# Optimization experiments

Hardware: AMD Instinct MI355X
Metric: run time of the kernel (lower is better)

Reference implementation:

```python
import jax, jax.numpy as jnp
import numpy as np

BSZ, L, P, H = 8, 8192, 128, 128


def setup_inputs() -> dict:
    key = jax.random.key(0)
    ks = jax.random.split(key, 7)
    x = jax.random.normal(ks[0], (BSZ, L, H), jnp.float32)
    A_diag = jax.random.uniform(ks[1], (P,), jnp.float32, 0.0, 2.0)
    G_diag = jax.random.uniform(ks[2], (P,), jnp.float32, 0.0, 1.0)
    dt = jax.random.normal(ks[3], (P,), jnp.float32)
    B = jax.random.uniform(ks[4], (P, H, 2), jnp.float32, -1.0, 1.0) / np.sqrt(H)
    C = jax.random.uniform(ks[5], (H, P, 2), jnp.float32, -1.0, 1.0) / np.sqrt(P)
    D = jax.random.normal(ks[6], (H,), jnp.float32)
    return {"x": x, "A_diag": A_diag, "G_diag": G_diag, "dt": dt, "B": B, "C": C, "D": D}


def _project_G(G, A, dt):
    # clamp G >= 0 and fold A into the valid stability interval [A_low, A_high]
    G = jnp.maximum(G, 0.0)
    dt2 = jnp.maximum(dt ** 2, 1e-06)
    s = jnp.sqrt(1.0 + dt * G)
    A_low = (2.0 + dt * G - 2.0 * s) / dt2
    A_high = (2.0 + dt * G + 2.0 * s) / dt2
    A_proj = A_low + jax.nn.relu(A - A_low) - jax.nn.relu(A - A_high)
    return A_proj, G


def _binop(q_i, q_j):
    # 2x2 block (per diagonal state p) recurrence composition: M_j @ M_i
    A_i, b_i = q_i
    A_j, b_j = q_j
    A_new = jnp.einsum('...ikp,...kjp->...ijp', A_j, A_i)
    b_new = jnp.einsum('...ikp,...kp->...ip', A_j, b_i) + b_j
    return A_new, b_new


def reference(x, A_diag, G_diag, dt, B, C, D):
    # _project_A_dt
    dt_s = jax.nn.sigmoid(dt)                       # (P,)
    A = jnp.maximum(A_diag, 0.0)
    # G_base = projected G given (A, dt)
    _, G_base = _project_G(G_diag, A, dt_s)
    # constant damping: G_seq is G_base broadcast over time, then re-projected per step
    G_seq = jnp.broadcast_to(G_base, (L, P))        # (L,P)
    A_seq, G_seq = _project_G(G_seq, A, dt_s)       # broadcasts over L
    A_fin = jnp.min(A_seq, axis=0)                  # (P,)
    # complex input projection Bu_k = B_complex @ u_k
    Bc = B[..., 0] + 1j * B[..., 1]                 # (P,H)
    Cc = C[..., 0] + 1j * C[..., 1]                 # (H,P)
    Bu = jnp.einsum('blh,ph->blp', x, Bc)           # (BSZ,L,P) complex64
    # IMEX transition coefficients
    S = 1.0 + dt_s * G_seq                          # (L,P)
    M11 = 1.0 / S
    M12 = -(dt_s / S) * A_fin
    M21 = dt_s / S
    M22 = 1.0 - (dt_s ** 2 / S) * A_fin
    M = jnp.stack([jnp.stack([M11, M12], axis=-2),
                   jnp.stack([M21, M22], axis=-2)], axis=-3)   # (L,2,2,P) real
    F = jnp.stack([(dt_s / S) * Bu, (dt_s ** 2 / S) * Bu], axis=-2)  # (BSZ,L,2,P) complex
    M_b = jnp.broadcast_to(M, (BSZ,) + M.shape)     # (BSZ,L,2,2,P)
    _, xs = jax.lax.associative_scan(_binop, (M_b, F), axis=1)
    ys = xs[..., 1, :]                              # (BSZ,L,P) complex: x-component
    out = jnp.einsum('blp,hp->blh', ys, Cc).real + D * x
    return out
```

## Files before the change

### kernel.cpp

```cpp
#include <hip/hip_runtime.h>
#include <math.h>

#define BSZ_ 8
#define LEN_ 8192
#define NC_  128
#define CT_  64

typedef __attribute__((ext_vector_type(8))) short bf16x8;
typedef __attribute__((ext_vector_type(4))) float f32x4;

#define OFF_PRM 0
#define OFF_W1T 2048
#define OFF_W2T (OFF_W1T + 16384)
#define OFF_SUM (OFF_W2T + 16384)

__device__ __forceinline__ unsigned short f2bf(float f) {
    unsigned u = __builtin_bit_cast(unsigned, f);
    u += 0x7fffu + ((u >> 16) & 1u);
    return (unsigned short)(u >> 16);
}

__global__ __launch_bounds__(256) void k_setup(const float* __restrict__ A_diag,
                                               const float* __restrict__ G_diag,
                                               const float* __restrict__ dt,
                                               const float* __restrict__ B,
                                               const float* __restrict__ C,
                                               float* __restrict__ ws)
{
    int i = blockIdx.x * 256 + threadIdx.x;
    {
        int pc = i >> 7, h = i & 127;
        int p = pc >> 1, cc = pc & 1;
        float dts = 1.f / (1.f + expf(-dt[p]));
        float G = fmaxf(G_diag[p], 0.f);
        float c1 = dts / (1.f + dts * G);
        ((unsigned short*)(ws + OFF_W1T))[i] = f2bf(c1 * B[p * 256 + h * 2 + cc]);
    }
    {
        float v = C[i];
        ((unsigned short*)(ws + OFF_W2T))[i] = f2bf((i & 1) ? -v : v);
    }
    if (blockIdx.x == 0 && threadIdx.x < 128) {
        int p = threadIdx.x;
        float dtv = dt[p];
        float dts = 1.f / (1.f + expf(-dtv));
        float A   = fmaxf(A_diag[p], 0.f);
        float G   = fmaxf(G_diag[p], 0.f);
        float dt2 = fmaxf(dts * dts, 1e-6f);
        float s   = sqrtf(1.f + dts * G);
        float A_low  = (2.f + dts * G - 2.f * s) / dt2;
        float A_high = (2.f + dts * G + 2.f * s) / dt2;
        float Af = A_low + fmaxf(A - A_low, 0.f) - fmaxf(A - A_high, 0.f);
        float S   = 1.f + dts * G;
        float M11 = 1.f / S;
        float M12 = -(dts / S) * Af;
        float M21 = dts / S;
        float M22 = 1.f - (dts * dts / S) * Af;
        float t11 = M11, t12 = M12, t21 = M21, t22 = M22;
#pragma unroll
        for (int it = 0; it < 6; ++it) {
            float n11 = t11 * t11 + t12 * t21;
            float n12 = t11 * t12 + t12 * t22;
            float n21 = t21 * t11 + t22 * t21;
            float n22 = t21 * t12 + t22 * t22;
            t11 = n11; t12 = n12; t21 = n21; t22 = n22;
        }
        float* prm = ws + OFF_PRM + p * 16;
        prm[0] = M11; prm[1] = M12; prm[2] = M21; prm[3] = M22; prm[4] = dts;
        prm[5] = t11; prm[6] = t12; prm[7] = t21; prm[8] = t22;
    }
}

__device__ __forceinline__ void stage_x(const float* __restrict__ X, size_t row0,
                                        int tid, unsigned short (*xs)[136])
{
    int r = tid >> 4, cl = (tid & 15) * 8;
#pragma unroll
    for (int i = 0; i < 4; ++i) {
        int rr = r + i * 16;
        const float* src = X + (row0 + rr) * 128 + cl;
        float4 v0 = *(const float4*)src;
        float4 v1 = *(const float4*)(src + 4);
        unsigned short* dst = &xs[rr][cl];
        dst[0] = f2bf(v0.x); dst[1] = f2bf(v0.y); dst[2] = f2bf(v0.z); dst[3] = f2bf(v0.w);
        dst[4] = f2bf(v1.x); dst[5] = f2bf(v1.y); dst[6] = f2bf(v1.z); dst[7] = f2bf(v1.w);
    }
}

__device__ __forceinline__ void gemm1_acc(const unsigned short (*xs)[136],
                                          const unsigned short* __restrict__ W1T,
                                          int wv, int lane, f32x4 acc[4][4])
{
    int l15 = lane & 15, quad = lane >> 4;
    int nbase = wv * 64;
#pragma unroll
    for (int kk = 0; kk < 4; ++kk) {
        int k0 = kk * 32 + quad * 8;
        bf16x8 af[4], bg[4];
#pragma unroll
        for (int mi = 0; mi < 4; ++mi) af[mi] = *(const bf16x8*)&xs[mi * 16 + l15][k0];
#pragma unroll
        for (int nj = 0; nj < 4; ++nj)
            bg[nj] = *(const bf16x8*)(W1T + (size_t)(nbase + nj * 16 + l15) * 128 + k0);
#pragma unroll
        for (int mi = 0; mi < 4; ++mi)
#pragma unroll
            for (int nj = 0; nj < 4; ++nj)
                acc[mi][nj] = __builtin_amdgcn_mfma_f32_16x16x32_bf16(af[mi], bg[nj], acc[mi][nj], 0, 0, 0);
    }
}

__global__ __launch_bounds__(256) void k_fuse1(const float* __restrict__ X,
                                               float* __restrict__ ws)
{
    __shared__ __align__(16) char smem[64 * 258 * 4];
    unsigned short (*xs)[136] = (unsigned short (*)[136])smem;
    float (*fl)[258] = (float (*)[258])smem;

    int tid = threadIdx.x;
    int b = blockIdx.x >> 7, c = blockIdx.x & 127;
    size_t row0 = (size_t)b * LEN_ + (size_t)c * CT_;

    stage_x(X, row0, tid, xs);
    __syncthreads();

    int wv = tid >> 6, lane = tid & 63;
    int l15 = lane & 15, quad = lane >> 4, nbase = wv * 64;
    f32x4 acc[4][4] = {};
    gemm1_acc(xs, (const unsigned short*)(ws + OFF_W1T), wv, lane, acc);
    __syncthreads();

#pragma unroll
    for (int mi = 0; mi < 4; ++mi)
#pragma unroll
        for (int nj = 0; nj < 4; ++nj)
#pragma unroll
            for (int r = 0; r < 4; ++r)
                fl[mi * 16 + quad * 4 + r][nbase + nj * 16 + l15] = acc[mi][nj][r];
    __syncthreads();

    const float* prm = ws + OFF_PRM + (tid >> 1) * 16;
    float M11 = prm[0], M12 = prm[1], M21 = prm[2], M22 = prm[3], dts = prm[4];
    float h1 = 0.f, h2 = 0.f;
#pragma unroll 8
    for (int t = 0; t < CT_; ++t) {
        float u = fl[t][tid];
        float n1 = fmaf(M11, h1, fmaf(M12, h2, u));
        float n2 = fmaf(M21, h1, fmaf(M22, h2, dts * u));
        h1 = n1; h2 = n2;
    }
    *(float2*)(ws + OFF_SUM + (((size_t)b * NC_ + c) * 256 + tid) * 2) = make_float2(h1, h2);
}

__global__ __launch_bounds__(64) void k_scan2(float* __restrict__ ws)
{
    int b = blockIdx.x >> 2, cg = blockIdx.x & 3;
    int ch = cg * 64 + threadIdx.x;
    const float* prm = ws + OFF_PRM + (ch >> 1) * 16;
    float T11 = prm[5], T12 = prm[6], T21 = prm[7], T22 = prm[8];
    float e1 = 0.f, e2 = 0.f;
    float* base = ws + OFF_SUM + (size_t)b * 65536 + ch * 2;
#pragma unroll 8
    for (int j = 0; j < NC_; ++j) {
        float2 l = *(float2*)(base + (size_t)j * 512);
        *(float2*)(base + (size_t)j * 512) = make_float2(e1, e2);
        float n1 = fmaf(T11, e1, fmaf(T12, e2, l.x));
        float n2 = fmaf(T21, e1, fmaf(T22, e2, l.y));
        e1 = n1; e2 = n2;
    }
}

__global__ __launch_bounds__(256) void k_fuse2(const float* __restrict__ X,
                                               const float* __restrict__ Dv,
                                               float* __restrict__ ws,
                                               float* __restrict__ out)
{
    __shared__ __align__(16) char smem[64 * 260 * 4];
    unsigned short (*xs)[136] = (unsigned short (*)[136])smem;
    float (*fl)[260]          = (float (*)[260])smem;
    __shared__ __align__(16) unsigned short ysb[64][264];

    int tid = threadIdx.x;
    int b = blockIdx.x >> 7, c = blockIdx.x & 127;
    size_t row0 = (size_t)b * LEN_ + (size_t)c * CT_;

    stage_x(X, row0, tid, xs);
    __syncthreads();

    int wv = tid >> 6, lane = tid & 63;
    int l15 = lane & 15, quad = lane >> 4, nbase = wv * 64;
    {
        f32x4 acc[4][4] = {};
        gemm1_acc(xs, (const unsigned short*)(ws + OFF_W1T), wv, lane, acc);
        __syncthreads();
#pragma unroll
        for (int mi = 0; mi < 4; ++mi)
#pragma unroll
            for (int nj = 0; nj < 4; ++nj)
#pragma unroll
                for (int r = 0; r < 4; ++r)
                    fl[mi * 16 + quad * 4 + r][nbase + nj * 16 + l15] = acc[mi][nj][r];
    }
    __syncthreads();

    {
        const float* prm = ws + OFF_PRM + (tid >> 1) * 16;
        float M11 = prm[0], M12 = prm[1], M21 = prm[2], M22 = prm[3], dts = prm[4];
        float2 s = *(const float2*)(ws + OFF_SUM + (((size_t)b * NC_ + c) * 256 + tid) * 2);
        float h1 = s.x, h2 = s.y;
#pragma unroll 8
        for (int t = 0; t < CT_; ++t) {
            float u = fl[t][tid];
            float n1 = fmaf(M11, h1, fmaf(M12, h2, u));
            float n2 = fmaf(M21, h1, fmaf(M22, h2, dts * u));
            h1 = n1; h2 = n2;
            ysb[t][tid] = f2bf(h2);
        }
    }
    __syncthreads();

    int mrow = (wv & 1) * 32, ncol = (wv >> 1) * 64;
    f32x4 a2[2][4] = {};
    const unsigned short* W2T = (const unsigned short*)(ws + OFF_W2T);
#pragma unroll
    for (int kk = 0; kk < 8; ++kk) {
        int k0 = kk * 32 + quad * 8;
        bf16x8 af[2], bg[4];
#pragma unroll
        for (int mi = 0; mi < 2; ++mi) af[mi] = *(const bf16x8*)&ysb[mrow + mi * 16 + l15][k0];
#pragma unroll
        for (int nj = 0; nj < 4; ++nj)
            bg[nj] = *(const bf16x8*)(W2T + (size_t)(ncol + nj * 16 + l15) * 256 + k0);
#pragma unroll
        for (int mi = 0; mi < 2; ++mi)
#pragma unroll
            for (int nj = 0; nj < 4; ++nj)
                a2[mi][nj] = __builtin_amdgcn_mfma_f32_16x16x32_bf16(af[mi], bg[nj], a2[mi][nj], 0, 0, 0);
    }

#pragma unroll
    for (int mi = 0; mi < 2; ++mi)
#pragma unroll
        for (int nj = 0; nj < 4; ++nj) {
            int col = ncol + nj * 16 + l15;
            float d = Dv[col];
#pragma unroll
            for (int r = 0; r < 4; ++r) {
                size_t gr = row0 + mrow + mi * 16 + quad * 4 + r;
                float xv = X[gr * 128 + col];
                out[gr * 128 + col] = fmaf(d, xv, a2[mi][nj][r]);
            }
        }
}

extern "C" void kernel_launch(void* const* d_in, const int* in_sizes, int n_in,
                              void* d_out, int out_size, void* d_ws, size_t ws_size,
                              hipStream_t stream) {
    const float* x      = (const float*)d_in[0];
    const float* A_diag = (const float*)d_in[1];
    const float* G_diag = (const float*)d_in[2];
    const float* dt     = (const float*)d_in[3];
    const float* B      = (const float*)d_in[4];
    const float* C      = (const float*)d_in[5];
    const float* Dv     = (const float*)d_in[6];
    float* out = (float*)d_out;
    float* ws  = (float*)d_ws;

    k_setup<<<128, 256, 0, stream>>>(A_diag, G_diag, dt, B, C, ws);
    k_fuse1<<<BSZ_ * NC_, 256, 0, stream>>>(x, ws);
    k_scan2<<<32, 64, 0, stream>>>(ws);
    k_fuse2<<<BSZ_ * NC_, 256, 0, stream>>>(x, Dv, ws, out);
}
```

Baseline: 151.5 us.

## Store zero-state chunk scan outputs and apply carry-in correction via precomputed matrix powers

The first pass now writes the zero-initial-state scan output h2 for every timestep to a global workspace. It also shrinks the shared buffer by processing the chunk in two halves. The second pass no longer recomputes the input GEMM and the sequential scan. Instead it adds the carry-in contribution through precomputed rows of M^k built in setup, which makes it a parallel elementwise pass. This removes duplicated GEMM and serial scan work but adds a large fp32 global write and read of per-step states.

Result: faster. 148.1 us (-2.2%).

```diff
diff --git a/kernel.cpp b/kernel.cpp
--- a/kernel.cpp
+++ b/kernel.cpp
@@ -12,7 +12,9 @@
 #define OFF_PRM 0
 #define OFF_W1T 2048
 #define OFF_W2T (OFF_W1T + 16384)
-#define OFF_SUM (OFF_W2T + 16384)
+#define OFF_MPW (OFF_W2T + 16384)
+#define OFF_SUM (OFF_MPW + 16640)
+#define OFF_V2  (OFF_SUM + BSZ_*NC_*256*2)
 
 __device__ __forceinline__ unsigned short f2bf(float f) {
     unsigned u = __builtin_bit_cast(unsigned, f);
@@ -68,6 +70,17 @@
         float* prm = ws + OFF_PRM + p * 16;
         prm[0] = M11; prm[1] = M12; prm[2] = M21; prm[3] = M22; prm[4] = dts;
         prm[5] = t11; prm[6] = t12; prm[7] = t21; prm[8] = t22;
+
+        float2* MPW = (float2*)(ws + OFF_MPW);
+        float c11 = M11, c12 = M12, c21 = M21, c22 = M22;
+        for (int k = 1; k <= 64; ++k) {
+            MPW[k * 128 + p] = make_float2(c21, c22);
+            float n11 = M11 * c11 + M12 * c21;
+            float n12 = M11 * c12 + M12 * c22;
+            float n21 = M21 * c11 + M22 * c21;
+            float n22 = M21 * c12 + M22 * c22;
+            c11 = n11; c12 = n12; c21 = n21; c22 = n22;
+        }
     }
 }
 
@@ -113,9 +126,9 @@
 __global__ __launch_bounds__(256) void k_fuse1(const float* __restrict__ X,
                                                float* __restrict__ ws)
 {
-    __shared__ __align__(16) char smem[64 * 258 * 4];
+    __shared__ __align__(16) char smem[32 * 260 * 4];
     unsigned short (*xs)[136] = (unsigned short (*)[136])smem;
-    float (*fl)[258] = (float (*)[258])smem;
+    float (*fl)[260] = (float (*)[260])smem;
 
     int tid = threadIdx.x;
     int b = blockIdx.x >> 7, c = blockIdx.x & 127;
@@ -130,24 +143,31 @@
     gemm1_acc(xs, (const unsigned short*)(ws + OFF_W1T), wv, lane, acc);
     __syncthreads();
 
-#pragma unroll
-    for (int mi = 0; mi < 4; ++mi)
-#pragma unroll
-        for (int nj = 0; nj < 4; ++nj)
-#pragma unroll
-            for (int r = 0; r < 4; ++r)
-                fl[mi * 16 + quad * 4 + r][nbase + nj * 16 + l15] = acc[mi][nj][r];
-    __syncthreads();
-
     const float* prm = ws + OFF_PRM + (tid >> 1) * 16;
     float M11 = prm[0], M12 = prm[1], M21 = prm[2], M22 = prm[3], dts = prm[4];
+    float* V2 = ws + OFF_V2;
     float h1 = 0.f, h2 = 0.f;
+
+#pragma unroll
+    for (int half = 0; half < 2; ++half) {
+#pragma unroll
+        for (int mi = 0; mi < 2; ++mi)
+#pragma unroll
+            for (int nj = 0; nj < 4; ++nj)
+#pragma unroll
+                for (int r = 0; r < 4; ++r)
+                    fl[mi * 16 + quad * 4 + r][nbase + nj * 16 + l15] =
+                        acc[half * 2 + mi][nj][r];
+        __syncthreads();
 #pragma unroll 8
-    for (int t = 0; t < CT_; ++t) {
-        float u = fl[t][tid];
-        float n1 = fmaf(M11, h1, fmaf(M12, h2, u));
-        float n2 = fmaf(M21, h1, fmaf(M22, h2, dts * u));
-        h1 = n1; h2 = n2;
+        for (int t = 0; t < 32; ++t) {
+            float u = fl[t][tid];
+            float n1 = fmaf(M11, h1, fmaf(M12, h2, u));
+            float n2 = fmaf(M21, h1, fmaf(M22, h2, dts * u));
+            h1 = n1; h2 = n2;
+            V2[(row0 + half * 32 + t) * 256 + tid] = h2;
+        }
+        __syncthreads();
     }
     *(float2*)(ws + OFF_SUM + (((size_t)b * NC_ + c) * 256 + tid) * 2) = make_float2(h1, h2);
 }
@@ -175,50 +195,29 @@
                                                float* __restrict__ ws,
                                                float* __restrict__ out)
 {
-    __shared__ __align__(16) char smem[64 * 260 * 4];
-    unsigned short (*xs)[136] = (unsigned short (*)[136])smem;
-    float (*fl)[260]          = (float (*)[260])smem;
     __shared__ __align__(16) unsigned short ysb[64][264];
 
     int tid = threadIdx.x;
     int b = blockIdx.x >> 7, c = blockIdx.x & 127;
     size_t row0 = (size_t)b * LEN_ + (size_t)c * CT_;
 
-    stage_x(X, row0, tid, xs);
+    {
+        int p = tid >> 1;
+        float2 C = *(const float2*)(ws + OFF_SUM + (((size_t)b * NC_ + c) * 256 + tid) * 2);
+        const float2* MPW = (const float2*)(ws + OFF_MPW);
+        const float* V2 = ws + OFF_V2 + row0 * 256 + tid;
+#pragma unroll 8
+        for (int t = 0; t < 64; ++t) {
+            float v2 = V2[(size_t)t * 256];
+            float2 m = MPW[(t + 1) * 128 + p];
+            float y = fmaf(m.x, C.x, fmaf(m.y, C.y, v2));
+            ysb[t][tid] = f2bf(y);
+        }
+    }
     __syncthreads();
 
     int wv = tid >> 6, lane = tid & 63;
-    int l15 = lane & 15, quad = lane >> 4, nbase = wv * 64;
-    {
-        f32x4 acc[4][4] = {};
-        gemm1_acc(xs, (const unsigned short*)(ws + OFF_W1T), wv, lane, acc);
-        __syncthreads();
-#pragma unroll
-        for (int mi = 0; mi < 4; ++mi)
-#pragma unroll
-            for (int nj = 0; nj < 4; ++nj)
-#pragma unroll
-                for (int r = 0; r < 4; ++r)
-                    fl[mi * 16 + quad * 4 + r][nbase + nj * 16 + l15] = acc[mi][nj][r];
-    }
-    __syncthreads();
-
-    {
-        const float* prm = ws + OFF_PRM + (tid >> 1) * 16;
-        float M11 = prm[0], M12 = prm[1], M21 = prm[2], M22 = prm[3], dts = prm[4];
-        float2 s = *(const float2*)(ws + OFF_SUM + (((size_t)b * NC_ + c) * 256 + tid) * 2);
-        float h1 = s.x, h2 = s.y;
-#pragma unroll 8
-        for (int t = 0; t < CT_; ++t) {
-            float u = fl[t][tid];
-            float n1 = fmaf(M11, h1, fmaf(M12, h2, u));
-            float n2 = fmaf(M21, h1, fmaf(M22, h2, dts * u));
-            h1 = n1; h2 = n2;
-            ysb[t][tid] = f2bf(h2);
-        }
-    }
-    __syncthreads();
-
+    int l15 = lane & 15, quad = lane >> 4;
     int mrow = (wv & 1) * 32, ncol = (wv >> 1) * 64;
     f32x4 a2[2][4] = {};
     const unsigned short* W2T = (const unsigned short*)(ws + OFF_W2T);
```
